# Kernel tuning notes

Measured on AMD Instinct MI355X. Metric: run time of the kernel, lower is better.

## Reference

```python
import jax, jax.numpy as jnp
import numpy as np

EMBED_DIM = 512
NUM_HEADS = 8
NUM_RULES = 16
HEAD_DIM = EMBED_DIM // NUM_HEADS


def setup_inputs() -> dict:
    key = jax.random.key(0)
    ks = jax.random.split(key, 10)
    B, S, E, H, R, D = 4, 2048, EMBED_DIM, NUM_HEADS, NUM_RULES, HEAD_DIM
    lim_q = 1.0 / np.sqrt(E)
    lim_v = 1.0 / np.sqrt(E)
    return {
        "query": jax.random.normal(ks[0], (B, S, E), jnp.float32),
        "key": jax.random.normal(ks[1], (B, S, E), jnp.float32),
        "value": jax.random.normal(ks[2], (B, S, E), jnp.float32),
        "Wq": jax.random.uniform(ks[3], (E, E), jnp.float32, -lim_q, lim_q),
        "bq": jax.random.uniform(ks[4], (E,), jnp.float32, -lim_q, lim_q),
        "Wv": jax.random.uniform(ks[5], (E * R, E), jnp.float32, -lim_v, lim_v),
        "bv": jax.random.uniform(ks[6], (E * R,), jnp.float32, -lim_v, lim_v),
        "Wo": jax.random.uniform(ks[7], (E, E), jnp.float32, -lim_q, lim_q),
        "bo": jax.random.uniform(ks[8], (E,), jnp.float32, -lim_q, lim_q),
        "rules_keys": 0.02 * jax.random.normal(ks[9], (H, R, D), jnp.float32),
        "rules_widths": jnp.ones((H, R, D), jnp.float32),
    }


def reference(query, key, value, Wq, bq, Wv, bv, Wo, bo, rules_keys, rules_widths):
    B, S, E = query.shape
    H, R, D = NUM_HEADS, NUM_RULES, HEAD_DIM
    scale = D ** -0.5
    # preprocessing_query: Linear + scale, split heads -> (b, h, s, d)
    q = (query @ Wq.T + bq) * scale
    q = q.reshape(B, S, H, D).transpose(0, 2, 1, 3)
    # custom_distance (l1): |q - rule_key| broadcast over rules -> (b, h, s, r, d)
    diff = jnp.abs(q[:, :, :, None, :] - rules_keys[None, :, None, :, :])
    # get_z_values: z = mean_d( -0.5 * (diff / width)^2 ) -> (b, h, s, r)
    z = -0.5 * jnp.mean(jnp.square(diff / rules_widths[None, :, None, :, :]), axis=-1)
    # softmax over rules (last dim), dropout is identity (p=0)
    attn = jax.nn.softmax(z, axis=-1)  # (b, h, s, r)
    # preprocessing_value: Linear(E -> E*R) + scale, 'b s (h d r) -> b s h d r'
    v = (value @ Wv.T + bv) * scale
    v = v.reshape(B, S, H, D, R)
    # Fnn_output = attn * v summed over rules -> (b, s, h, d)
    out = jnp.einsum("bhsr,bshdr->bshd", attn, v)
    # torch: (b,s,h,d).transpose(1,2).contiguous().view(b, -1, h*d)
    out = out.transpose(0, 2, 1, 3).reshape(B, -1, H * D)
    return out @ Wo.T + bo
```

## Files before the change

kernel.cpp:

```cpp
#include <hip/hip_runtime.h>
#include <stdint.h>

#define TOKENS 8192
#define EDIM 512
#define HNUM 8
#define RNUM 16
#define DDIM 64
#define KDIM 512

typedef short v8s __attribute__((ext_vector_type(8)));
typedef float v4f __attribute__((ext_vector_type(4)));

__device__ inline float b2f(unsigned short u) {
    union { unsigned int i; float f; } c; c.i = ((unsigned int)u) << 16; return c.f;
}
__device__ inline unsigned short f2b(float f) {
    union { float f; unsigned int i; } c; c.f = f;
    unsigned int i = c.i + 0x7fffu + ((c.i >> 16) & 1u);
    return (unsigned short)(i >> 16);
}

#define GLD16(dst, src) \
    __builtin_amdgcn_global_load_lds((__attribute__((address_space(1))) void*)(src), \
                                     (__attribute__((address_space(3))) void*)(dst), 16, 0, 0)

__global__ __launch_bounds__(256)
void cvt5(const float* __restrict__ s0, const float* __restrict__ s1,
          const float* __restrict__ s2, const float* __restrict__ s3,
          const float* __restrict__ s4,
          unsigned short* __restrict__ d0, unsigned short* __restrict__ d1,
          unsigned short* __restrict__ d2, unsigned short* __restrict__ d3,
          unsigned short* __restrict__ d4,
          int n0, int n1, int n2, int n3, int n4)
{
    const float* s; unsigned short* d; int n;
    switch (blockIdx.y) {
        case 0: s = s0; d = d0; n = n0; break;
        case 1: s = s1; d = d1; n = n1; break;
        case 2: s = s2; d = d2; n = n2; break;
        case 3: s = s3; d = d3; n = n3; break;
        default: s = s4; d = d4; n = n4; break;
    }
    size_t base = (size_t)blockIdx.x * 2048 + (size_t)threadIdx.x * 8;
    if (base >= (size_t)n) return;
    const float4* sp = (const float4*)(s + base);
    float4 f0 = sp[0], f1 = sp[1];
    v8s o;
    o[0] = (short)f2b(f0.x); o[1] = (short)f2b(f0.y);
    o[2] = (short)f2b(f0.z); o[3] = (short)f2b(f0.w);
    o[4] = (short)f2b(f1.x); o[5] = (short)f2b(f1.y);
    o[6] = (short)f2b(f1.z); o[7] = (short)f2b(f1.w);
    *(v8s*)(d + base) = o;
}

template <int MODE>
__global__ __launch_bounds__(256, 4)
void gemm64(const unsigned short* __restrict__ A,
            const unsigned short* __restrict__ B,
            const float* __restrict__ bias,
            float* __restrict__ outF,
            unsigned short* __restrict__ outH)
{
    __shared__ unsigned short As[64 * 32];
    __shared__ unsigned short Bs[64 * 32];

    const int tid  = threadIdx.x;
    const int w    = tid >> 6;
    const int lane = tid & 63;
    const int quad = lane >> 4;
    const int l16  = lane & 15;
    const int wm   = w >> 1, wn = w & 1;
    const int m0   = blockIdx.x * 64;
    const int n0   = blockIdx.y * 64;

    v4f acc[2][2];
#pragma unroll
    for (int i = 0; i < 2; ++i)
#pragma unroll
        for (int j = 0; j < 2; ++j)
            acc[i][j] = (v4f){0.f, 0.f, 0.f, 0.f};

    for (int kt = 0; kt < KDIM / 32; ++kt) {
        int c = w * 64 + lane;
        const unsigned short* sa = A + (size_t)(m0 + (c >> 2)) * KDIM + kt * 32 + (c & 3) * 8;
        GLD16(&As[w * 512], sa);
        const unsigned short* sb = B + (size_t)(n0 + (c >> 2)) * KDIM + kt * 32 + (c & 3) * 8;
        GLD16(&Bs[w * 512], sb);
        __syncthreads();

        v8s af[2], bf[2];
#pragma unroll
        for (int mt = 0; mt < 2; ++mt)
            af[mt] = *(const v8s*)&As[(wm * 32 + mt * 16 + l16) * 32 + quad * 8];
#pragma unroll
        for (int nt = 0; nt < 2; ++nt)
            bf[nt] = *(const v8s*)&Bs[(wn * 32 + nt * 16 + l16) * 32 + quad * 8];
#pragma unroll
        for (int mt = 0; mt < 2; ++mt)
#pragma unroll
            for (int nt = 0; nt < 2; ++nt)
                acc[mt][nt] = __builtin_amdgcn_mfma_f32_16x16x32_bf16(af[mt], bf[nt], acc[mt][nt], 0, 0, 0);
        __syncthreads();
    }

#pragma unroll
    for (int mt = 0; mt < 2; ++mt)
#pragma unroll
        for (int nt = 0; nt < 2; ++nt) {
            int col = n0 + wn * 32 + nt * 16 + l16;
            float bb = bias[col];
#pragma unroll
            for (int rg = 0; rg < 4; ++rg) {
                int row = m0 + wm * 32 + mt * 16 + quad * 4 + rg;
                float v = acc[mt][nt][rg] + bb;
                if (MODE == 0) outH[(size_t)row * EDIM + col] = f2b(v * 0.125f);
                else           outF[(size_t)row * EDIM + col] = v;
            }
        }
}

__device__ __forceinline__ v8s ldfrag(const unsigned short* base, int r, int g) {
    return *(const v8s*)(base + (r << 6) + ((g ^ (r & 7)) << 3));
}

#define MEMBAR asm volatile("" ::: "memory")
#define BARX do { MEMBAR; __builtin_amdgcn_s_barrier(); MEMBAR; } while (0)
#define WAITV(n) asm volatile("s_waitcnt vmcnt(" #n ")" ::: "memory")

#define STAGE_H(ldsArr, bufi, half_, gptr, rowbase, ktv) do { \
    const unsigned short* s_ = (gptr) + (size_t)((rowbase) + (half_) * 128 + (w << 4) + rsub) * KDIM \
                               + (ktv) * 64 + (gsw << 3); \
    GLD16(&ldsArr[bufi][(half_) * 8192 + (w << 10)], s_); \
    GLD16(&ldsArr[bufi][(half_) * 8192 + (w << 10) + 512], s_ + 8 * KDIM); \
} while (0)

#define LDA8(mq_) do { \
    _Pragma("unroll") \
    for (int mi = 0; mi < 4; ++mi) \
        _Pragma("unroll") \
        for (int ks = 0; ks < 2; ++ks) \
            af[mi * 2 + ks] = ldfrag(abase, wm * 64 + (mq_) * 128 + mi * 16 + l16, ks * 4 + quad); \
} while (0)

#define LDB4(nq_, dst) do { \
    _Pragma("unroll") \
    for (int ni = 0; ni < 2; ++ni) \
        _Pragma("unroll") \
        for (int ks = 0; ks < 2; ++ks) \
            dst[ni * 2 + ks] = ldfrag(bbase, wn * 32 + (nq_) * 128 + ni * 16 + l16, ks * 4 + quad); \
} while (0)

#define MFMA16(ai_, bfr) do { \
    __builtin_amdgcn_s_setprio(1); \
    _Pragma("unroll") \
    for (int ks = 0; ks < 2; ++ks) \
        _Pragma("unroll") \
        for (int mi = 0; mi < 4; ++mi) \
            _Pragma("unroll") \
            for (int ni = 0; ni < 2; ++ni) \
                acc[ai_][mi][ni] = __builtin_amdgcn_mfma_f32_16x16x32_bf16( \
                    af[mi * 2 + ks], bfr[ni * 2 + ks], acc[ai_][mi][ni], 0, 0, 0); \
    __builtin_amdgcn_s_setprio(0); \
} while (0)

__global__ __launch_bounds__(512, 2)
void gemm_v(const unsigned short* __restrict__ A,
            const unsigned short* __restrict__ B,
            const float* __restrict__ bias,
            unsigned short* __restrict__ outH,
            const float* __restrict__ attn)
{
    __shared__ unsigned short As[2][16384];
    __shared__ unsigned short Bs[2][16384];

    const int tid  = threadIdx.x;
    const int w    = tid >> 6;
    const int lane = tid & 63;
    const int quad = lane >> 4;
    const int l16  = lane & 15;
    const int wm   = w >> 2;
    const int wn   = w & 3;
    const int rsub = lane >> 3;
    const int gsw  = (lane & 7) ^ rsub;

    const int c  = blockIdx.x & 7;
    const int j  = blockIdx.x >> 3;
    const int mb = (j & 7) | ((j >> 5) << 3);
    const int nb = (j >> 3) & 3;
    const int m0 = mb << 8;
    const int n0 = (c * 4 + nb) << 8;

    v4f acc[4][4][2];
#pragma unroll
    for (int q = 0; q < 4; ++q)
#pragma unroll
        for (int mi = 0; mi < 4; ++mi)
#pragma unroll
            for (int ni = 0; ni < 2; ++ni)
                acc[q][mi][ni] = (v4f){0.f, 0.f, 0.f, 0.f};

    v8s af[8], bf0[4], bf1[4];

    STAGE_H(As, 0, 0, A, m0, 0);
    STAGE_H(Bs, 0, 0, B, n0, 0);
    STAGE_H(As, 0, 1, A, m0, 0);
    STAGE_H(Bs, 0, 1, B, n0, 0);
    STAGE_H(As, 1, 0, A, m0, 1);
    STAGE_H(Bs, 1, 1, B, n0, 1);
    WAITV(4);
    BARX;

#pragma unroll
    for (int T = 0; T < KDIM / 64; ++T) {
        const unsigned short* abase = &As[T & 1][0];
        const unsigned short* bbase = &Bs[T & 1][0];
        const int ob = (T & 1) ^ 1;

        LDA8(0); LDB4(0, bf0);
        if (T < 7) STAGE_H(As, ob, 1, A, m0, T + 1);
        MFMA16(0, bf0);
        LDB4(1, bf1);
        if (T < 7) STAGE_H(Bs, ob, 0, B, n0, T + 1);
        MFMA16(1, bf1);
        BARX;

        LDA8(1);
        if (T < 6) STAGE_H(As, T & 1, 0, A, m0, T + 2);
        MFMA16(3, bf1);
        if (T < 6) STAGE_H(Bs, T & 1, 1, B, n0, T + 2);
        MFMA16(2, bf0);
        if (T < 6) { WAITV(4); } else { WAITV(0); }
        BARX;
    }

    unsigned short* Osp = &As[0][0];
    const int h  = m0 >> 10;
    const int d0 = (m0 >> 4) & 63;
#pragma unroll
    for (int mq = 0; mq < 2; ++mq)
#pragma unroll
        for (int nq = 0; nq < 2; ++nq)
#pragma unroll
            for (int mi = 0; mi < 4; ++mi) {
                float4 bias4 = *(const float4*)&bias[m0 + mq * 128 + wm * 64 + mi * 16 + quad * 4];
#pragma unroll
                for (int ni = 0; ni < 2; ++ni) {
                    int tloc  = nq * 128 + wn * 32 + ni * 16 + l16;
                    float4 av = *(const float4*)&attn[(size_t)(n0 + tloc) * (HNUM * RNUM) + h * RNUM + quad * 4];
                    v4f a = acc[mq * 2 + nq][mi][ni];
                    float val = (a[0] + bias4.x) * av.x + (a[1] + bias4.y) * av.y
                              + (a[2] + bias4.z) * av.z + (a[3] + bias4.w) * av.w;
                    val += __shfl_xor(val, 16);
                    val += __shfl_xor(val, 32);
                    if (quad == 0)
                        Osp[tloc * 16 + (mq * 8 + wm * 4 + mi)] = f2b(val * 0.125f);
                }
            }
    __syncthreads();
    {
        int tl = tid >> 1, hf = tid & 1;
        int sg = n0 + tl;
        int g  = (sg >> 11) * 2048 + h * 256 + ((sg & 2047) >> 3);
        int jx = (sg & 7) * 64 + d0 + hf * 8;
        *(v8s*)&outH[(size_t)g * EDIM + jx] = *(const v8s*)&Osp[tl * 16 + hf * 8];
    }
}

#define RST 72
__global__ __launch_bounds__(256)
void rules_softmax(const unsigned short* __restrict__ q,
                   const float* __restrict__ rk,
                   const float* __restrict__ rw,
                   float* __restrict__ attn)
{
    __shared__ float ql[16 * RST];
    __shared__ float rkl[16 * RST];
    __shared__ float iwl[16 * RST];
    const int h   = blockIdx.y;
    const int t0  = blockIdx.x * 16;
    const int tid = threadIdx.x;

#pragma unroll
    for (int i = 0; i < 4; ++i) {
        int jj = tid + i * 256;
        int r = jj >> 6, d = jj & 63;
        rkl[r * RST + d] = rk[h * (RNUM * DDIM) + jj];
        float wv = rw[h * (RNUM * DDIM) + jj];
        iwl[r * RST + d] = 1.0f / (wv * wv);
    }
    {
        int jj = tid * 4;
        int row = jj >> 6, d = jj & 63;
        const unsigned short* src = q + (size_t)(t0 + row) * EDIM + h * DDIM + d;
        unsigned short u0 = src[0], u1 = src[1], u2 = src[2], u3 = src[3];
        ql[row * RST + d + 0] = b2f(u0);
        ql[row * RST + d + 1] = b2f(u1);
        ql[row * RST + d + 2] = b2f(u2);
        ql[row * RST + d + 3] = b2f(u3);
    }
    __syncthreads();

    const int tl = tid >> 4;
    const int r  = tid & 15;
    const float* qrow = &ql[tl * RST];
    const float* krow = &rkl[r * RST];
    const float* wrow = &iwl[r * RST];
    float z = 0.f;
#pragma unroll
    for (int d4 = 0; d4 < 16; ++d4) {
        float4 qv = *(const float4*)&qrow[d4 * 4];
        float4 kv = *(const float4*)&krow[d4 * 4];
        float4 wv = *(const float4*)&wrow[d4 * 4];
        float a0 = qv.x - kv.x; z += a0 * a0 * wv.x;
        float a1 = qv.y - kv.y; z += a1 * a1 * wv.y;
        float a2 = qv.z - kv.z; z += a2 * a2 * wv.z;
        float a3 = qv.w - kv.w; z += a3 * a3 * wv.w;
    }
    z *= (-0.5f / 64.f);
    float mx = z;
#pragma unroll
    for (int s = 1; s < 16; s <<= 1) mx = fmaxf(mx, __shfl_xor(mx, s));
    float e = __expf(z - mx);
    float sum = e;
#pragma unroll
    for (int s = 1; s < 16; s <<= 1) sum += __shfl_xor(sum, s);
    attn[(size_t)(t0 + tl) * (HNUM * RNUM) + h * RNUM + r] = e / sum;
}

extern "C" void kernel_launch(void* const* d_in, const int* in_sizes, int n_in,
                              void* d_out, int out_size, void* d_ws, size_t ws_size,
                              hipStream_t stream) {
    const float* query = (const float*)d_in[0];
    const float* value = (const float*)d_in[2];
    const float* Wq = (const float*)d_in[3];
    const float* bq = (const float*)d_in[4];
    const float* Wv = (const float*)d_in[5];
    const float* bv = (const float*)d_in[6];
    const float* Wo = (const float*)d_in[7];
    const float* bo = (const float*)d_in[8];
    const float* rk = (const float*)d_in[9];
    const float* rw = (const float*)d_in[10];

    char* ws = (char*)d_ws;
    unsigned short* qbf  = (unsigned short*)(ws);
    unsigned short* vbf  = (unsigned short*)(ws + (size_t)( 8 << 20));
    unsigned short* Wqb  = (unsigned short*)(ws + (size_t)(16 << 20));
    unsigned short* Wvb  = (unsigned short*)(ws + (size_t)(17 << 20));
    unsigned short* Wob  = (unsigned short*)(ws + (size_t)(25 << 20));
    unsigned short* out1 = (unsigned short*)(ws + (size_t)(26 << 20));
    unsigned short* qf   = (unsigned short*)(ws + (size_t)(34 << 20));
    float* attn          = (float*)(ws + (size_t)(42 << 20));

    dim3 blk(256);
    cvt5<<<dim3(2048, 5), blk, 0, stream>>>(query, value, Wv, Wq, Wo,
                                            qbf, vbf, Wvb, Wqb, Wob,
                                            TOKENS * EDIM, TOKENS * EDIM, EDIM * RNUM * EDIM,
                                            EDIM * EDIM, EDIM * EDIM);
    gemm64<0><<<dim3(TOKENS / 64, EDIM / 64), blk, 0, stream>>>(qbf, Wqb, bq, nullptr, qf);
    rules_softmax<<<dim3(TOKENS / 16, HNUM), blk, 0, stream>>>(qf, rk, rw, attn);
    gemm_v<<<dim3(1024), dim3(512), 0, stream>>>(Wvb, vbf, bv, out1, attn);
    gemm64<2><<<dim3(TOKENS / 64, EDIM / 64), blk, 0, stream>>>(out1, Wob, bo, (float*)d_out, nullptr);
}
```

Measured before the change: 227.3 us.

## Make value GEMM persistent over four N tiles with triple-buffered K=32 stages

The value-projection GEMM now launches 256 blocks instead of 1024. Each block loops over four consecutive 256-token N tiles, running a single continuous pipeline across them. The K step shrinks to 32 with a three-deep LDS ring and a new swizzled fragment layout. The attention-weighted epilogue runs after every 16 K steps, so the prologue and pipeline fill cost is amortized and tile switching overlaps the next tile's loads. The risks are fewer blocks for the GPU's CUs, more barriers per unit of work, and a non-unrolled loop with runtime buffer selection.

Measured after the change: 231.8 us. No clear change (+2.0%).

```diff
diff --git a/kernel.cpp b/kernel.cpp
--- a/kernel.cpp
+++ b/kernel.cpp
@@ -120,47 +120,19 @@
 }
 
 __device__ __forceinline__ v8s ldfrag(const unsigned short* base, int r, int g) {
-    return *(const v8s*)(base + (r << 6) + ((g ^ (r & 7)) << 3));
+    return *(const v8s*)(base + ((r >> 1) << 6) + ((((g << 1) | (r & 1)) ^ ((r >> 1) & 7)) << 3));
 }
 
 #define MEMBAR asm volatile("" ::: "memory")
 #define BARX do { MEMBAR; __builtin_amdgcn_s_barrier(); MEMBAR; } while (0)
+#define BARL do { MEMBAR; asm volatile("s_waitcnt lgkmcnt(0)" ::: "memory"); \
+                  __builtin_amdgcn_s_barrier(); MEMBAR; } while (0)
 #define WAITV(n) asm volatile("s_waitcnt vmcnt(" #n ")" ::: "memory")
 
-#define STAGE_H(ldsArr, bufi, half_, gptr, rowbase, ktv) do { \
-    const unsigned short* s_ = (gptr) + (size_t)((rowbase) + (half_) * 128 + (w << 4) + rsub) * KDIM \
-                               + (ktv) * 64 + (gsw << 3); \
-    GLD16(&ldsArr[bufi][(half_) * 8192 + (w << 10)], s_); \
-    GLD16(&ldsArr[bufi][(half_) * 8192 + (w << 10) + 512], s_ + 8 * KDIM); \
-} while (0)
-
-#define LDA8(mq_) do { \
-    _Pragma("unroll") \
-    for (int mi = 0; mi < 4; ++mi) \
-        _Pragma("unroll") \
-        for (int ks = 0; ks < 2; ++ks) \
-            af[mi * 2 + ks] = ldfrag(abase, wm * 64 + (mq_) * 128 + mi * 16 + l16, ks * 4 + quad); \
-} while (0)
-
-#define LDB4(nq_, dst) do { \
-    _Pragma("unroll") \
-    for (int ni = 0; ni < 2; ++ni) \
-        _Pragma("unroll") \
-        for (int ks = 0; ks < 2; ++ks) \
-            dst[ni * 2 + ks] = ldfrag(bbase, wn * 32 + (nq_) * 128 + ni * 16 + l16, ks * 4 + quad); \
-} while (0)
-
-#define MFMA16(ai_, bfr) do { \
-    __builtin_amdgcn_s_setprio(1); \
-    _Pragma("unroll") \
-    for (int ks = 0; ks < 2; ++ks) \
-        _Pragma("unroll") \
-        for (int mi = 0; mi < 4; ++mi) \
-            _Pragma("unroll") \
-            for (int ni = 0; ni < 2; ++ni) \
-                acc[ai_][mi][ni] = __builtin_amdgcn_mfma_f32_16x16x32_bf16( \
-                    af[mi * 2 + ks], bfr[ni * 2 + ks], acc[ai_][mi][ni], 0, 0, 0); \
-    __builtin_amdgcn_s_setprio(0); \
+#define STAGE_T(bufp, gptr, grow0, k0s) do { \
+    const unsigned short* s_ = (gptr) + (size_t)((grow0) + (w << 5) + rloc) * KDIM + (k0s) + gidx * 8; \
+    GLD16((bufp) + (w << 10), s_); \
+    GLD16((bufp) + (w << 10) + 512, s_ + 16 * KDIM); \
 } while (0)
 
 __global__ __launch_bounds__(512, 2)
@@ -170,8 +142,9 @@
             unsigned short* __restrict__ outH,
             const float* __restrict__ attn)
 {
-    __shared__ unsigned short As[2][16384];
-    __shared__ unsigned short Bs[2][16384];
+    __shared__ unsigned short As3[3][8192];
+    __shared__ unsigned short Bs3[3][8192];
+    __shared__ unsigned short Os[4096];
 
     const int tid  = threadIdx.x;
     const int w    = tid >> 6;
@@ -180,15 +153,16 @@
     const int l16  = lane & 15;
     const int wm   = w >> 2;
     const int wn   = w & 3;
-    const int rsub = lane >> 3;
-    const int gsw  = (lane & 7) ^ rsub;
+    const int su   = (lane & 7) ^ ((lane >> 3) & 7);
+    const int rloc = ((lane >> 3) << 1) | (su & 1);
+    const int gidx = su >> 1;
 
     const int c  = blockIdx.x & 7;
     const int j  = blockIdx.x >> 3;
-    const int mb = (j & 7) | ((j >> 5) << 3);
-    const int nb = (j >> 3) & 3;
-    const int m0 = mb << 8;
-    const int n0 = (c * 4 + nb) << 8;
+    const int mb = ((c & 3) << 3) | (j & 7);
+    const int ng = ((c >> 2) << 2) | (j >> 3);
+    const int m0  = mb << 8;
+    const int n0b = ng << 10;
 
     v4f acc[4][4][2];
 #pragma unroll
@@ -199,70 +173,102 @@
             for (int ni = 0; ni < 2; ++ni)
                 acc[q][mi][ni] = (v4f){0.f, 0.f, 0.f, 0.f};
 
-    v8s af[8], bf0[4], bf1[4];
-
-    STAGE_H(As, 0, 0, A, m0, 0);
-    STAGE_H(Bs, 0, 0, B, n0, 0);
-    STAGE_H(As, 0, 1, A, m0, 0);
-    STAGE_H(Bs, 0, 1, B, n0, 0);
-    STAGE_H(As, 1, 0, A, m0, 1);
-    STAGE_H(Bs, 1, 1, B, n0, 1);
+    const int h  = m0 >> 10;
+    const int d0 = (m0 >> 4) & 63;
+
+    STAGE_T(&As3[0][0], A, m0, 0);
+    STAGE_T(&Bs3[0][0], B, n0b, 0);
+    STAGE_T(&As3[1][0], A, m0, 32);
+    STAGE_T(&Bs3[1][0], B, n0b, 32);
     WAITV(4);
     BARX;
 
-#pragma unroll
-    for (int T = 0; T < KDIM / 64; ++T) {
-        const unsigned short* abase = &As[T & 1][0];
-        const unsigned short* bbase = &Bs[T & 1][0];
-        const int ob = (T & 1) ^ 1;
-
-        LDA8(0); LDB4(0, bf0);
-        if (T < 7) STAGE_H(As, ob, 1, A, m0, T + 1);
-        MFMA16(0, bf0);
-        LDB4(1, bf1);
-        if (T < 7) STAGE_H(Bs, ob, 0, B, n0, T + 1);
-        MFMA16(1, bf1);
+    int cur = 0;
+#pragma unroll 1
+    for (int G = 0; G < 64; ++G) {
+        const unsigned short* abase = (cur == 0) ? &As3[0][0] : (cur == 1) ? &As3[1][0] : &As3[2][0];
+        const unsigned short* bbase = (cur == 0) ? &Bs3[0][0] : (cur == 1) ? &Bs3[1][0] : &Bs3[2][0];
+
+        v8s af[8], bf[4];
+#pragma unroll
+        for (int mq = 0; mq < 2; ++mq)
+#pragma unroll
+            for (int mi = 0; mi < 4; ++mi)
+                af[mq * 4 + mi] = ldfrag(abase, mq * 128 + wm * 64 + mi * 16 + l16, quad);
+#pragma unroll
+        for (int nq = 0; nq < 2; ++nq)
+#pragma unroll
+            for (int ni = 0; ni < 2; ++ni)
+                bf[nq * 2 + ni] = ldfrag(bbase, nq * 128 + wn * 32 + ni * 16 + l16, quad);
+
+        if (G < 62) {
+            const int G2  = G + 2;
+            const int stg = (cur == 0) ? 2 : cur - 1;
+            unsigned short* sa = (stg == 0) ? &As3[0][0] : (stg == 1) ? &As3[1][0] : &As3[2][0];
+            unsigned short* sb = (stg == 0) ? &Bs3[0][0] : (stg == 1) ? &Bs3[1][0] : &Bs3[2][0];
+            const int k0s = (G2 & 15) * 32;
+            const int n0s = n0b + ((G2 >> 4) << 8);
+            STAGE_T(sa, A, m0, k0s);
+            STAGE_T(sb, B, n0s, k0s);
+        }
+
+        __builtin_amdgcn_s_setprio(1);
+#pragma unroll
+        for (int mq = 0; mq < 2; ++mq)
+#pragma unroll
+            for (int nq = 0; nq < 2; ++nq)
+#pragma unroll
+                for (int mi = 0; mi < 4; ++mi)
+#pragma unroll
+                    for (int ni = 0; ni < 2; ++ni)
+                        acc[mq * 2 + nq][mi][ni] = __builtin_amdgcn_mfma_f32_16x16x32_bf16(
+                            af[mq * 4 + mi], bf[nq * 2 + ni], acc[mq * 2 + nq][mi][ni], 0, 0, 0);
+        __builtin_amdgcn_s_setprio(0);
+
+        if (G < 62) { WAITV(4); } else { WAITV(0); }
         BARX;
 
-        LDA8(1);
-        if (T < 6) STAGE_H(As, T & 1, 0, A, m0, T + 2);
-        MFMA16(3, bf1);
-        if (T < 6) STAGE_H(Bs, T & 1, 1, B, n0, T + 2);
-        MFMA16(2, bf0);
-        if (T < 6) { WAITV(4); } else { WAITV(0); }
-        BARX;
-    }
-
-    unsigned short* Osp = &As[0][0];
-    const int h  = m0 >> 10;
-    const int d0 = (m0 >> 4) & 63;
-#pragma unroll
-    for (int mq = 0; mq < 2; ++mq)
-#pragma unroll
-        for (int nq = 0; nq < 2; ++nq)
-#pragma unroll
-            for (int mi = 0; mi < 4; ++mi) {
-                float4 bias4 = *(const float4*)&bias[m0 + mq * 128 + wm * 64 + mi * 16 + quad * 4];
-#pragma unroll
-                for (int ni = 0; ni < 2; ++ni) {
-                    int tloc  = nq * 128 + wn * 32 + ni * 16 + l16;
-                    float4 av = *(const float4*)&attn[(size_t)(n0 + tloc) * (HNUM * RNUM) + h * RNUM + quad * 4];
-                    v4f a = acc[mq * 2 + nq][mi][ni];
-                    float val = (a[0] + bias4.x) * av.x + (a[1] + bias4.y) * av.y
-                              + (a[2] + bias4.z) * av.z + (a[3] + bias4.w) * av.w;
-                    val += __shfl_xor(val, 16);
-                    val += __shfl_xor(val, 32);
-                    if (quad == 0)
-                        Osp[tloc * 16 + (mq * 8 + wm * 4 + mi)] = f2b(val * 0.125f);
-                }
+        if ((G & 15) == 15) {
+            const int n0t = n0b + ((G >> 4) << 8);
+#pragma unroll
+            for (int mq = 0; mq < 2; ++mq)
+#pragma unroll
+                for (int nq = 0; nq < 2; ++nq)
+#pragma unroll
+                    for (int mi = 0; mi < 4; ++mi) {
+                        float4 bias4 = *(const float4*)&bias[m0 + mq * 128 + wm * 64 + mi * 16 + quad * 4];
+#pragma unroll
+                        for (int ni = 0; ni < 2; ++ni) {
+                            int tloc  = nq * 128 + wn * 32 + ni * 16 + l16;
+                            float4 av = *(const float4*)&attn[(size_t)(n0t + tloc) * (HNUM * RNUM) + h * RNUM + quad * 4];
+                            v4f a = acc[mq * 2 + nq][mi][ni];
+                            float val = (a[0] + bias4.x) * av.x + (a[1] + bias4.y) * av.y
+                                      + (a[2] + bias4.z) * av.z + (a[3] + bias4.w) * av.w;
+                            val += __shfl_xor(val, 16);
+                            val += __shfl_xor(val, 32);
+                            if (quad == 0)
+                                Os[tloc * 16 + (mq * 8 + wm * 4 + mi)] = f2b(val * 0.125f);
+                        }
+                    }
+            BARL;
+            {
+                int tl = tid >> 1, hf = tid & 1;
+                int sg = n0t + tl;
+                int g  = (sg >> 11) * 2048 + h * 256 + ((sg & 2047) >> 3);
+                int jx = (sg & 7) * 64 + d0 + hf * 8;
+                *(v8s*)&outH[(size_t)g * EDIM + jx] = *(const v8s*)&Os[tl * 16 + hf * 8];
             }
-    __syncthreads();
-    {
-        int tl = tid >> 1, hf = tid & 1;
-        int sg = n0 + tl;
-        int g  = (sg >> 11) * 2048 + h * 256 + ((sg & 2047) >> 3);
-        int jx = (sg & 7) * 64 + d0 + hf * 8;
-        *(v8s*)&outH[(size_t)g * EDIM + jx] = *(const v8s*)&Osp[tl * 16 + hf * 8];
+            if (G < 63) {
+#pragma unroll
+                for (int q = 0; q < 4; ++q)
+#pragma unroll
+                    for (int mi = 0; mi < 4; ++mi)
+#pragma unroll
+                        for (int ni = 0; ni < 2; ++ni)
+                            acc[q][mi][ni] = (v4f){0.f, 0.f, 0.f, 0.f};
+            }
+        }
+        cur = (cur == 2) ? 0 : cur + 1;
     }
 }
 
@@ -358,6 +364,6 @@
                                             EDIM * EDIM, EDIM * EDIM);
     gemm64<0><<<dim3(TOKENS / 64, EDIM / 64), blk, 0, stream>>>(qbf, Wqb, bq, nullptr, qf);
     rules_softmax<<<dim3(TOKENS / 16, HNUM), blk, 0, stream>>>(qf, rk, rw, attn);
-    gemm_v<<<dim3(1024), dim3(512), 0, stream>>>(Wvb, vbf, bv, out1, attn);
+    gemm_v<<<dim3(256), dim3(512), 0, stream>>>(Wvb, vbf, bv, out1, attn);
     gemm64<2><<<dim3(TOKENS / 64, EDIM / 64), blk, 0, stream>>>(out1, Wob, bo, (float*)d_out, nullptr);
 }
```
